# Performance work log

Measured on AMD Instinct MI355X. Metric: run time of the kernel, lower is better.

Reference implementation:

```python
import jax, jax.numpy as jnp
import numpy as np

D_MODEL = 1024
D_STATE = 16
D_CONV = 4
EXPAND = 2
D_INNER = D_MODEL * EXPAND
B = 1
L = 2048


def setup_inputs() -> dict:
    key = jax.random.key(0)
    ks = jax.random.split(key, 8)
    s = lambda k, shape, scale: jax.random.normal(k, shape, dtype=jnp.float32) * scale
    return {
        "x": jax.random.normal(ks[0], (B, L, D_MODEL), dtype=jnp.float32),
        "in_proj_w": s(ks[1], (D_INNER * 2, D_MODEL), D_MODEL ** -0.5),
        "conv_w": s(ks[2], (D_INNER, 1, D_CONV), D_CONV ** -0.5),  # depthwise [O, I/g=1, K]
        "conv_b": jnp.zeros((D_INNER,), jnp.float32),
        "x_proj_w": s(ks[3], (2 * D_STATE + 1, D_INNER), D_INNER ** -0.5),
        "dt_proj_w": s(ks[4], (D_INNER, 1), 1.0),
        "dt_proj_b": jnp.zeros((D_INNER,), jnp.float32),
        "A_log": jnp.log(jnp.broadcast_to(jnp.arange(1, D_STATE + 1, dtype=jnp.float32), (D_INNER, D_STATE))),
        "D": jnp.ones((D_INNER,), jnp.float32),
        "out_proj_w": s(ks[5], (D_MODEL, D_INNER), D_INNER ** -0.5),
    }


def reference(x, in_proj_w, conv_w, conv_b, x_proj_w, dt_proj_w, dt_proj_b, A_log, D, out_proj_w):
    Bb = x.shape[0]
    # in_proj -> split into ssm branch and gate z
    xz = x @ in_proj_w.T                      # [B, L, 2*Di]
    x_ssm, z = jnp.split(xz, 2, axis=-1)
    # causal depthwise conv1d (torch pads K-1 both sides then slices [:L] == left-pad K-1)
    xt = jnp.swapaxes(x_ssm, 1, 2)            # [B, Di, L]
    xc = jax.lax.conv_general_dilated(
        xt, conv_w, window_strides=(1,), padding=[(D_CONV - 1, 0)],
        feature_group_count=D_INNER, dimension_numbers=("NCH", "OIH", "NCH"))
    xc = xc + conv_b[None, :, None]
    xc = jax.nn.silu(jnp.swapaxes(xc, 1, 2))  # [B, L, Di]
    # selective SSM
    A = -jnp.exp(A_log)                        # [Di, N]
    xp = xc @ x_proj_w.T                       # [B, L, 1+2N]
    dt_r = xp[..., :1]
    Bv = xp[..., 1:1 + D_STATE]                # [B, L, N]
    Cv = xp[..., 1 + D_STATE:]                 # [B, L, N]
    dt = jax.nn.softplus(dt_r @ dt_proj_w.T + dt_proj_b)   # [B, L, Di]
    dA = jnp.exp(dt[..., None] * A)                          # [B, L, Di, N]
    dBx = dt[..., None] * Bv[:, :, None, :] * xc[..., None]  # [B, L, Di, N]

    def step(h, inps):
        dA_t, dBx_t, C_t = inps
        h = dA_t * h + dBx_t                   # [B, Di, N]
        y = jnp.einsum("bdn,bn->bd", h, C_t)
        return h, y

    h0 = jnp.zeros((Bb, D_INNER, D_STATE), x.dtype)
    _, ys = jax.lax.scan(step, h0, (jnp.swapaxes(dA, 0, 1), jnp.swapaxes(dBx, 0, 1), jnp.swapaxes(Cv, 0, 1)))
    y = jnp.swapaxes(ys, 0, 1) + xc * D        # [B, L, Di]
    return (y * jax.nn.silu(z)) @ out_proj_w.T
```

## Files before the change

kernel.cpp:

```cpp
#include <hip/hip_runtime.h>
#include <math.h>

#define L_SEQ   2048
#define DM      1024
#define DI      2048
#define NST     16
#define LC      32
#define NCHUNK  64
#define XP_LD   36
#define KSPLIT  8
#define LOG2E   1.44269504f

typedef short s16x8 __attribute__((ext_vector_type(8)));
typedef unsigned short u16x8 __attribute__((ext_vector_type(8)));
typedef float f32x4 __attribute__((ext_vector_type(4)));

__device__ __forceinline__ float silu_f(float x) {
  return x / (1.0f + __expf(-x));
}
__device__ __forceinline__ float softplus_f(float x) {
  return x > 20.0f ? x : __logf(1.0f + __expf(x));
}
__device__ __forceinline__ ushort f2bf(float f) {
  unsigned int u = __float_as_uint(f);
  unsigned int r = (u + 0x7fffu + ((u >> 16) & 1u)) >> 16;
  return (ushort)r;
}
__device__ __forceinline__ float bf2f(ushort u) {
  return __uint_as_float((unsigned int)u << 16);
}
__device__ __forceinline__ void gload_lds16(const void* g, void* lds) {
  __builtin_amdgcn_global_load_lds(
      (const __attribute__((address_space(1))) unsigned int*)g,
      (__attribute__((address_space(3))) unsigned int*)lds,
      16, 0, 0);
}

__global__ __launch_bounds__(256) void cvt_bf16_k(
    const float* __restrict__ in, ushort* __restrict__ out, int n4) {
  int i = blockIdx.x * 256 + threadIdx.x;
  if (i >= n4) return;
  float4 v = ((const float4*)in)[i];
  ushort4 o;
  o.x = f2bf(v.x); o.y = f2bf(v.y); o.z = f2bf(v.z); o.w = f2bf(v.w);
  ((ushort4*)out)[i] = o;
}

template <int MFRAG, bool BF16OUT>
__global__ __launch_bounds__(256) void gemm_mfma_bf16(
    const ushort* __restrict__ A, const ushort* __restrict__ B,
    void* __restrict__ Cv, int K, int ldc) {
  constexpr int BM = MFRAG * 32;
  __shared__ ushort As[BM * 32];
  __shared__ ushort Bs[128 * 32];
  const int tid  = threadIdx.x;
  const int lane = tid & 63;
  const int wv   = tid >> 6;
  const int wr   = wv >> 1;
  const int wc   = wv & 1;
  const int m0 = blockIdx.y * BM;
  const int n0 = blockIdx.x * 128;

  f32x4 acc[MFRAG][4] = {};
  const int kc = (tid & 3) * 8;

  for (int k0 = 0; k0 < K; k0 += 32) {
    __syncthreads();
#pragma unroll
    for (int q = 0; q < BM / 64; ++q) {
      int id = q * 256 + tid;
      int m  = id >> 2;
      gload_lds16(A + (size_t)(m0 + m) * K + k0 + kc, (char*)As + id * 16);
    }
#pragma unroll
    for (int q = 0; q < 2; ++q) {
      int id = q * 256 + tid;
      int n  = id >> 2;
      gload_lds16(B + (size_t)(n0 + n) * K + k0 + kc, (char*)Bs + id * 16);
    }
    __syncthreads();

    s16x8 af[MFRAG], bfr[4];
#pragma unroll
    for (int m = 0; m < MFRAG; ++m)
      af[m] = *(const s16x8*)&As[(wr * MFRAG * 16 + m * 16 + (lane & 15)) * 32 + (lane >> 4) * 8];
#pragma unroll
    for (int n = 0; n < 4; ++n)
      bfr[n] = *(const s16x8*)&Bs[(wc * 64 + n * 16 + (lane & 15)) * 32 + (lane >> 4) * 8];
#pragma unroll
    for (int m = 0; m < MFRAG; ++m)
#pragma unroll
      for (int n = 0; n < 4; ++n)
        acc[m][n] = __builtin_amdgcn_mfma_f32_16x16x32_bf16(af[m], bfr[n], acc[m][n], 0, 0, 0);
  }
  const int cr = (lane >> 4) * 4;
  const int cc = lane & 15;
#pragma unroll
  for (int m = 0; m < MFRAG; ++m) {
    int gr0 = m0 + wr * MFRAG * 16 + m * 16 + cr;
#pragma unroll
    for (int n = 0; n < 4; ++n) {
      int gc = n0 + wc * 64 + n * 16 + cc;
#pragma unroll
      for (int r = 0; r < 4; ++r) {
        if constexpr (BF16OUT)
          ((ushort*)Cv)[(size_t)(gr0 + r) * ldc + gc] = f2bf(acc[m][n][r]);
        else
          ((float*)Cv)[(size_t)(gr0 + r) * ldc + gc] = acc[m][n][r];
      }
    }
  }
}

__global__ __launch_bounds__(256) void conv_silu_T_k(
    const ushort* __restrict__ xzb, const float* __restrict__ cw,
    const float* __restrict__ cb, float* __restrict__ xcT) {
  const int d0  = blockIdx.x * 64;
  const int l0  = blockIdx.y * 64;
  const int tid = threadIdx.x;
  __shared__ ushort xt[67][64];
  __shared__ float  ot[64][65];
#pragma unroll
  for (int q = 0; q < 3; ++q) {
    int id = q * 256 + tid;
    if (id < 67 * 8) {
      int row = id >> 3, c8 = (id & 7) * 8;
      int l = l0 - 3 + row;
      u16x8 v = (u16x8)(ushort)0;
      if (l >= 0)
        v = *(const u16x8*)&xzb[(size_t)l * 4096 + d0 + c8];
      *(u16x8*)&xt[row][c8] = v;
    }
  }
  __syncthreads();
  const int dloc = tid & 63;
  const int d    = d0 + dloc;
  const float w0 = cw[d*4+0], w1 = cw[d*4+1], w2 = cw[d*4+2], w3 = cw[d*4+3];
  const float bb = cb[d];
  const int lb = (tid >> 6) * 16;
#pragma unroll
  for (int j = 0; j < 16; ++j) {
    int ll = lb + j;
    float a = bb;
    a = fmaf(w0, bf2f(xt[ll+0][dloc]), a);
    a = fmaf(w1, bf2f(xt[ll+1][dloc]), a);
    a = fmaf(w2, bf2f(xt[ll+2][dloc]), a);
    a = fmaf(w3, bf2f(xt[ll+3][dloc]), a);
    ot[dloc][ll] = silu_f(a);
  }
  __syncthreads();
#pragma unroll
  for (int q = 0; q < 4; ++q) {
    int f4 = q * 256 + tid;
    int dr = f4 >> 4, lc = (f4 & 15) * 4;
    float4 v = make_float4(ot[dr][lc], ot[dr][lc+1], ot[dr][lc+2], ot[dr][lc+3]);
    *(float4*)&xcT[(size_t)(d0 + dr) * L_SEQ + l0 + lc] = v;
  }
}

__global__ __launch_bounds__(256) void gemm_xp_k(
    const float* __restrict__ xcT, const float* __restrict__ Wxp,
    float* __restrict__ xp_part) {
  const int L0   = blockIdx.x * 64;
  const int ks   = blockIdx.y;
  const int wv   = threadIdx.x >> 6;
  const int lane = threadIdx.x & 63;
  __shared__ float xcs[64][65];
  __shared__ float Ws[36][64];
  float acc[9] = {};
  const int kbeg = ks * (DI / KSPLIT);
  const int kend = kbeg + DI / KSPLIT;
  for (int k0 = kbeg; k0 < kend; k0 += 64) {
#pragma unroll
    for (int q = 0; q < 4; ++q) {
      int f4 = q * 256 + threadIdx.x;
      int dr = f4 >> 4;
      int lc = (f4 & 15) * 4;
      float4 v = *(const float4*)&xcT[(size_t)(k0 + dr) * L_SEQ + L0 + lc];
      xcs[lc+0][dr] = v.x; xcs[lc+1][dr] = v.y;
      xcs[lc+2][dr] = v.z; xcs[lc+3][dr] = v.w;
    }
    for (int idx = threadIdx.x; idx < 36 * 16; idx += 256) {
      int j = idx >> 4; int cc = (idx & 15) << 2;
      float4 v = make_float4(0.f, 0.f, 0.f, 0.f);
      if (j < 33) v = *(const float4*)&Wxp[(size_t)j * DI + k0 + cc];
      *(float4*)&Ws[j][cc] = v;
    }
    __syncthreads();
#pragma unroll 4
    for (int kk = 0; kk < 64; kk += 4) {
      float4 wr[9];
#pragma unroll
      for (int jj = 0; jj < 9; ++jj) wr[jj] = *(const float4*)&Ws[wv*9 + jj][kk];
      float a0 = xcs[lane][kk+0], a1 = xcs[lane][kk+1];
      float a2 = xcs[lane][kk+2], a3 = xcs[lane][kk+3];
#pragma unroll
      for (int jj = 0; jj < 9; ++jj) {
        acc[jj] = fmaf(a0, wr[jj].x, acc[jj]);
        acc[jj] = fmaf(a1, wr[jj].y, acc[jj]);
        acc[jj] = fmaf(a2, wr[jj].z, acc[jj]);
        acc[jj] = fmaf(a3, wr[jj].w, acc[jj]);
      }
    }
    __syncthreads();
  }
  const int l = L0 + lane;
#pragma unroll
  for (int jj = 0; jj < 9; ++jj) {
    int j = wv * 9 + jj;
    if (j < 33)
      xp_part[(size_t)ks * L_SEQ * XP_LD + (size_t)l * XP_LD + j] = acc[jj];
  }
}

__global__ __launch_bounds__(256) void reduce_xp_k(
    const float* __restrict__ part, float* __restrict__ xp) {
  int i = blockIdx.x * 256 + threadIdx.x;
  float s = 0.f;
#pragma unroll
  for (int ks = 0; ks < KSPLIT; ++ks)
    s += part[(size_t)ks * L_SEQ * XP_LD + i];
  xp[i] = s;
}

__device__ __forceinline__ void stage_xps(
    float (*xps)[36], const float* __restrict__ xp, int l0, int tid) {
  for (int idx = tid; idx < LC * 33; idx += 256) {
    int rr = idx / 33, j = idx - rr * 33;
    int col = (j == 0) ? 32 : j - 1;
    xps[rr][col] = xp[(size_t)(l0 + rr) * XP_LD + j];
  }
}
__device__ __forceinline__ void stage_xcs(
    float (*xcs)[LC + 1], const float* __restrict__ xcT, int d0, int l0, int tid) {
#pragma unroll
  for (int q = 0; q < 4; ++q) {
    int f4  = q * 256 + tid;
    int row = f4 >> 3;
    int col = (f4 & 7) * 4;
    float4 v = *(const float4*)&xcT[(size_t)(d0 + row) * L_SEQ + l0 + col];
    xcs[row][col+0] = v.x; xcs[row][col+1] = v.y;
    xcs[row][col+2] = v.z; xcs[row][col+3] = v.w;
  }
}
__device__ __forceinline__ void stage_dts(
    float (*dts)[128], float (*xps)[36],
    const float* __restrict__ dtw, const float* __restrict__ dtb,
    int d0, int tid) {
  int dd = tid & 127;
  int tb = (tid >> 7) * 16;
  float wv = dtw[d0 + dd], bv = dtb[d0 + dd];
#pragma unroll
  for (int j = 0; j < 16; ++j)
    dts[tb + j][dd] = softplus_f(fmaf(xps[tb + j][32], wv, bv));
}

__global__ __launch_bounds__(256) void scan_partial_k(
    const float* __restrict__ xcT, const float* __restrict__ xp,
    const float* __restrict__ dtw, const float* __restrict__ dtb,
    const float* __restrict__ A_log,
    float* __restrict__ P, float* __restrict__ Q) {
  const int tid = threadIdx.x;
  const int dl  = tid >> 1;
  const int d0  = blockIdx.x * 128;
  const int d   = d0 + dl;
  const int nb  = (tid & 1) * 8;
  const int c   = blockIdx.y;
  const int l0  = c * LC;
  __shared__ float xps[LC][36];
  __shared__ float xcs[128][LC + 1];
  __shared__ float dts[LC][128];
  stage_xps(xps, xp, l0, tid);
  stage_xcs(xcs, xcT, d0, l0, tid);

  float Ad2[8];
#pragma unroll
  for (int j4 = 0; j4 < 8; j4 += 4) {
    float4 v = *(const float4*)&A_log[(size_t)d * NST + nb + j4];
    Ad2[j4+0] = -__expf(v.x) * LOG2E; Ad2[j4+1] = -__expf(v.y) * LOG2E;
    Ad2[j4+2] = -__expf(v.z) * LOG2E; Ad2[j4+3] = -__expf(v.w) * LOG2E;
  }
  __syncthreads();
  stage_dts(dts, xps, dtw, dtb, d0, tid);
  float h[8];
#pragma unroll
  for (int n = 0; n < 8; ++n) h[n] = 0.f;
  float sumdt = 0.f;
  __syncthreads();
#pragma unroll 4
  for (int t = 0; t < LC; ++t) {
    float dt  = dts[t][dl];
    sumdt += dt;
    float dtx = dt * xcs[dl][t];
    f32x4 B0 = *(const f32x4*)&xps[t][nb];
    f32x4 B1 = *(const f32x4*)&xps[t][nb + 4];
    float Bv[8];
    *(f32x4*)&Bv[0] = B0; *(f32x4*)&Bv[4] = B1;
#pragma unroll
    for (int n = 0; n < 8; ++n) {
      float da = exp2f(dt * Ad2[n]);
      h[n] = fmaf(da, h[n], dtx * Bv[n]);
    }
  }
  float p[8];
#pragma unroll
  for (int n = 0; n < 8; ++n) p[n] = exp2f(sumdt * Ad2[n]);
  size_t base = ((size_t)c * DI + d) * NST + nb;
  *(float4*)&P[base]     = make_float4(p[0], p[1], p[2], p[3]);
  *(float4*)&P[base + 4] = make_float4(p[4], p[5], p[6], p[7]);
  *(float4*)&Q[base]     = make_float4(h[0], h[1], h[2], h[3]);
  *(float4*)&Q[base + 4] = make_float4(h[4], h[5], h[6], h[7]);
}

__global__ __launch_bounds__(256) void scan_prefix_k(
    const float* __restrict__ P, float* __restrict__ QHs) {
  const int g = blockIdx.x * 256 + threadIdx.x;
  const int d = g >> 2;
  const int q = (g & 3) << 2;
  float4 h = make_float4(0.f, 0.f, 0.f, 0.f);
#pragma unroll 8
  for (int c = 0; c < NCHUNK; ++c) {
    size_t base = ((size_t)c * DI + d) * NST + q;
    float4 pv = *(const float4*)&P[base];
    float4 qv = *(const float4*)&QHs[base];
    *(float4*)&QHs[base] = h;
    h.x = fmaf(pv.x, h.x, qv.x);
    h.y = fmaf(pv.y, h.y, qv.y);
    h.z = fmaf(pv.z, h.z, qv.z);
    h.w = fmaf(pv.w, h.w, qv.w);
  }
}

__global__ __launch_bounds__(256) void scan_final_k(
    const float* __restrict__ xcT, const float* __restrict__ xp,
    const float* __restrict__ dtw, const float* __restrict__ dtb,
    const float* __restrict__ A_log, const float* __restrict__ Dp,
    const float* __restrict__ Hs, const ushort* __restrict__ xzb,
    ushort* __restrict__ ys) {
  const int tid  = threadIdx.x;
  const int dl   = tid >> 1;
  const int d0   = blockIdx.x * 128;
  const int d    = d0 + dl;
  const int half = tid & 1;
  const int nb   = half * 8;
  const int c    = blockIdx.y;
  const int l0   = c * LC;
  __shared__ float  xps[LC][36];
  __shared__ float  xcs[128][LC + 1];
  __shared__ float  dts[LC][128];
  __shared__ ushort zs[LC][128];
#pragma unroll
  for (int q = 0; q < 2; ++q) {
    int id = q * 256 + tid;
    int t  = id >> 4;
    int c8 = (id & 15) * 8;
    gload_lds16(xzb + (size_t)(l0 + t) * 4096 + 2048 + d0 + c8,
                (char*)zs + id * 16);
  }
  stage_xps(xps, xp, l0, tid);
  stage_xcs(xcs, xcT, d0, l0, tid);

  float Ad2[8];
#pragma unroll
  for (int j4 = 0; j4 < 8; j4 += 4) {
    float4 v = *(const float4*)&A_log[(size_t)d * NST + nb + j4];
    Ad2[j4+0] = -__expf(v.x) * LOG2E; Ad2[j4+1] = -__expf(v.y) * LOG2E;
    Ad2[j4+2] = -__expf(v.z) * LOG2E; Ad2[j4+3] = -__expf(v.w) * LOG2E;
  }
  const float Dd = Dp[d];
  float h[8];
  size_t hb = ((size_t)c * DI + d) * NST + nb;
  *(float4*)&h[0] = *(const float4*)&Hs[hb];
  *(float4*)&h[4] = *(const float4*)&Hs[hb + 4];
  __syncthreads();
  stage_dts(dts, xps, dtw, dtb, d0, tid);
  __syncthreads();
#pragma unroll 4
  for (int t = 0; t < LC; ++t) {
    const int l = l0 + t;
    float dt  = dts[t][dl];
    float xcv = xcs[dl][t];
    float dtx = dt * xcv;
    f32x4 B0 = *(const f32x4*)&xps[t][nb];
    f32x4 B1 = *(const f32x4*)&xps[t][nb + 4];
    f32x4 C0 = *(const f32x4*)&xps[t][16 + nb];
    f32x4 C1 = *(const f32x4*)&xps[t][20 + nb];
    float Bv[8], Cv[8];
    *(f32x4*)&Bv[0] = B0; *(f32x4*)&Bv[4] = B1;
    *(f32x4*)&Cv[0] = C0; *(f32x4*)&Cv[4] = C1;
    float y = 0.f;
#pragma unroll
    for (int n = 0; n < 8; ++n) {
      float da = exp2f(dt * Ad2[n]);
      h[n] = fmaf(da, h[n], dtx * Bv[n]);
      y = fmaf(h[n], Cv[n], y);
    }
    y += __shfl_xor(y, 1);
    if (half == 0) {
      y = fmaf(xcv, Dd, y);
      ys[(size_t)l * DI + d] = f2bf(y * silu_f(bf2f(zs[t][dl])));
    }
  }
}

extern "C" void kernel_launch(void* const* d_in, const int* in_sizes, int n_in,
                              void* d_out, int out_size, void* d_ws, size_t ws_size,
                              hipStream_t stream) {
  const float* x    = (const float*)d_in[0];
  const float* W1   = (const float*)d_in[1];
  const float* cw   = (const float*)d_in[2];
  const float* cb   = (const float*)d_in[3];
  const float* Wxp  = (const float*)d_in[4];
  const float* dtw  = (const float*)d_in[5];
  const float* dtb  = (const float*)d_in[6];
  const float* Alog = (const float*)d_in[7];
  const float* Dp   = (const float*)d_in[8];
  const float* Wout = (const float*)d_in[9];
  float* out = (float*)d_out;

  char* w = (char*)d_ws;
  ushort* xz_bf   = (ushort*)w;
  float*  xcT     = (float*)(w + 16777216);
  ushort* x_bf    = (ushort*)(w + 33554432);
  ushort* W1_bf   = (ushort*)(w + 37748736);
  float*  P       = (float*)(w + 33554432);
  float*  QHs     = (float*)(w + 41943040);
  float*  xp      = (float*)(w + 50331648);
  ushort* Wout_bf = (ushort*)(w + 50626560);
  ushort* ys_bf   = (ushort*)(w + 54820864);
  float*  xp_part = (float*)(w + 54820864);

  cvt_bf16_k<<<2048, 256, 0, stream>>>(x,    x_bf,    2048*1024/4);
  cvt_bf16_k<<<4096, 256, 0, stream>>>(W1,   W1_bf,   4096*1024/4);
  cvt_bf16_k<<<2048, 256, 0, stream>>>(Wout, Wout_bf, 1024*2048/4);
  gemm_mfma_bf16<4, true><<<dim3(4096/128, 2048/128), 256, 0, stream>>>(
      x_bf, W1_bf, xz_bf, DM, 4096);
  conv_silu_T_k<<<dim3(DI/64, L_SEQ/64), 256, 0, stream>>>(xz_bf, cw, cb, xcT);
  gemm_xp_k<<<dim3(L_SEQ/64, KSPLIT), 256, 0, stream>>>(xcT, Wxp, xp_part);
  reduce_xp_k<<<L_SEQ*XP_LD/256, 256, 0, stream>>>(xp_part, xp);
  scan_partial_k<<<dim3(DI/128, NCHUNK), 256, 0, stream>>>(xcT, xp, dtw, dtb, Alog, P, QHs);
  scan_prefix_k<<<DI*NST/4/256, 256, 0, stream>>>(P, QHs);
  scan_final_k<<<dim3(DI/128, NCHUNK), 256, 0, stream>>>(xcT, xp, dtw, dtb, Alog, Dp, QHs, xz_bf, ys_bf);
  gemm_mfma_bf16<2, false><<<dim3(1024/128, 2048/64), 256, 0, stream>>>(
      ys_bf, Wout_bf, out, DI, 1024);
}
```

Baseline: 264.9 us.

## Split scan state across four lanes per channel and halve channel tile

```diff
diff --git a/kernel.cpp b/kernel.cpp
--- a/kernel.cpp
+++ b/kernel.cpp
@@ -231,10 +231,10 @@
     xps[rr][col] = xp[(size_t)(l0 + rr) * XP_LD + j];
   }
 }
-__device__ __forceinline__ void stage_xcs(
+__device__ __forceinline__ void stage_xcs64(
     float (*xcs)[LC + 1], const float* __restrict__ xcT, int d0, int l0, int tid) {
 #pragma unroll
-  for (int q = 0; q < 4; ++q) {
+  for (int q = 0; q < 2; ++q) {
     int f4  = q * 256 + tid;
     int row = f4 >> 3;
     int col = (f4 & 7) * 4;
@@ -243,48 +243,41 @@
     xcs[row][col+2] = v.z; xcs[row][col+3] = v.w;
   }
 }
-__device__ __forceinline__ void stage_dts(
-    float (*dts)[128], float (*xps)[36],
+__device__ __forceinline__ void stage_dts64(
+    float (*dts)[64], const float* __restrict__ xp,
     const float* __restrict__ dtw, const float* __restrict__ dtb,
-    int d0, int tid) {
-  int dd = tid & 127;
-  int tb = (tid >> 7) * 16;
+    int d0, int l0, int tid) {
+  int dd = tid & 63;
+  int tb = (tid >> 6) * 8;
   float wv = dtw[d0 + dd], bv = dtb[d0 + dd];
 #pragma unroll
-  for (int j = 0; j < 16; ++j)
-    dts[tb + j][dd] = softplus_f(fmaf(xps[tb + j][32], wv, bv));
-}
-
-__global__ __launch_bounds__(256) void scan_partial_k(
+  for (int j = 0; j < 8; ++j)
+    dts[tb + j][dd] = softplus_f(fmaf(xp[(size_t)(l0 + tb + j) * XP_LD], wv, bv));
+}
+
+__global__ __launch_bounds__(256, 4) void scan_partial_k(
     const float* __restrict__ xcT, const float* __restrict__ xp,
     const float* __restrict__ dtw, const float* __restrict__ dtb,
     const float* __restrict__ A_log,
     float* __restrict__ P, float* __restrict__ Q) {
   const int tid = threadIdx.x;
-  const int dl  = tid >> 1;
-  const int d0  = blockIdx.x * 128;
+  const int dl  = tid >> 2;
+  const int nq  = (tid & 3) * 4;
+  const int d0  = blockIdx.x * 64;
   const int d   = d0 + dl;
-  const int nb  = (tid & 1) * 8;
   const int c   = blockIdx.y;
   const int l0  = c * LC;
   __shared__ float xps[LC][36];
-  __shared__ float xcs[128][LC + 1];
-  __shared__ float dts[LC][128];
+  __shared__ float xcs[64][LC + 1];
+  __shared__ float dts[LC][64];
   stage_xps(xps, xp, l0, tid);
-  stage_xcs(xcs, xcT, d0, l0, tid);
-
-  float Ad2[8];
-#pragma unroll
-  for (int j4 = 0; j4 < 8; j4 += 4) {
-    float4 v = *(const float4*)&A_log[(size_t)d * NST + nb + j4];
-    Ad2[j4+0] = -__expf(v.x) * LOG2E; Ad2[j4+1] = -__expf(v.y) * LOG2E;
-    Ad2[j4+2] = -__expf(v.z) * LOG2E; Ad2[j4+3] = -__expf(v.w) * LOG2E;
-  }
-  __syncthreads();
-  stage_dts(dts, xps, dtw, dtb, d0, tid);
-  float h[8];
-#pragma unroll
-  for (int n = 0; n < 8; ++n) h[n] = 0.f;
+  stage_xcs64(xcs, xcT, d0, l0, tid);
+  stage_dts64(dts, xp, dtw, dtb, d0, l0, tid);
+
+  float4 Av = *(const float4*)&A_log[(size_t)d * NST + nq];
+  float Ad2[4] = { -__expf(Av.x) * LOG2E, -__expf(Av.y) * LOG2E,
+                   -__expf(Av.z) * LOG2E, -__expf(Av.w) * LOG2E };
+  float h[4] = {0.f, 0.f, 0.f, 0.f};
   float sumdt = 0.f;
   __syncthreads();
 #pragma unroll 4
@@ -292,24 +285,17 @@
     float dt  = dts[t][dl];
     sumdt += dt;
     float dtx = dt * xcs[dl][t];
-    f32x4 B0 = *(const f32x4*)&xps[t][nb];
-    f32x4 B1 = *(const f32x4*)&xps[t][nb + 4];
-    float Bv[8];
-    *(f32x4*)&Bv[0] = B0; *(f32x4*)&Bv[4] = B1;
-#pragma unroll
-    for (int n = 0; n < 8; ++n) {
+    f32x4 B = *(const f32x4*)&xps[t][nq];
+#pragma unroll
+    for (int n = 0; n < 4; ++n) {
       float da = exp2f(dt * Ad2[n]);
-      h[n] = fmaf(da, h[n], dtx * Bv[n]);
-    }
-  }
-  float p[8];
-#pragma unroll
-  for (int n = 0; n < 8; ++n) p[n] = exp2f(sumdt * Ad2[n]);
-  size_t base = ((size_t)c * DI + d) * NST + nb;
-  *(float4*)&P[base]     = make_float4(p[0], p[1], p[2], p[3]);
-  *(float4*)&P[base + 4] = make_float4(p[4], p[5], p[6], p[7]);
-  *(float4*)&Q[base]     = make_float4(h[0], h[1], h[2], h[3]);
-  *(float4*)&Q[base + 4] = make_float4(h[4], h[5], h[6], h[7]);
+      h[n] = fmaf(da, h[n], dtx * B[n]);
+    }
+  }
+  size_t base = ((size_t)c * DI + d) * NST + nq;
+  *(float4*)&P[base] = make_float4(exp2f(sumdt * Ad2[0]), exp2f(sumdt * Ad2[1]),
+                                   exp2f(sumdt * Ad2[2]), exp2f(sumdt * Ad2[3]));
+  *(float4*)&Q[base] = make_float4(h[0], h[1], h[2], h[3]);
 }
 
 __global__ __launch_bounds__(256) void scan_prefix_k(
@@ -331,49 +317,41 @@
   }
 }
 
-__global__ __launch_bounds__(256) void scan_final_k(
+__global__ __launch_bounds__(256, 4) void scan_final_k(
     const float* __restrict__ xcT, const float* __restrict__ xp,
     const float* __restrict__ dtw, const float* __restrict__ dtb,
     const float* __restrict__ A_log, const float* __restrict__ Dp,
     const float* __restrict__ Hs, const ushort* __restrict__ xzb,
     ushort* __restrict__ ys) {
-  const int tid  = threadIdx.x;
-  const int dl   = tid >> 1;
-  const int d0   = blockIdx.x * 128;
-  const int d    = d0 + dl;
-  const int half = tid & 1;
-  const int nb   = half * 8;
-  const int c    = blockIdx.y;
-  const int l0   = c * LC;
+  const int tid = threadIdx.x;
+  const int dl  = tid >> 2;
+  const int nq  = (tid & 3) * 4;
+  const int d0  = blockIdx.x * 64;
+  const int d   = d0 + dl;
+  const int c   = blockIdx.y;
+  const int l0  = c * LC;
   __shared__ float  xps[LC][36];
-  __shared__ float  xcs[128][LC + 1];
-  __shared__ float  dts[LC][128];
-  __shared__ ushort zs[LC][128];
-#pragma unroll
-  for (int q = 0; q < 2; ++q) {
-    int id = q * 256 + tid;
-    int t  = id >> 4;
-    int c8 = (id & 15) * 8;
+  __shared__ float  xcs[64][LC + 1];
+  __shared__ float  dts[LC][64];
+  __shared__ ushort zs[LC][64];
+  {
+    int id = tid;
+    int t  = id >> 3;
+    int c8 = (id & 7) * 8;
     gload_lds16(xzb + (size_t)(l0 + t) * 4096 + 2048 + d0 + c8,
                 (char*)zs + id * 16);
   }
   stage_xps(xps, xp, l0, tid);
-  stage_xcs(xcs, xcT, d0, l0, tid);
-
-  float Ad2[8];
-#pragma unroll
-  for (int j4 = 0; j4 < 8; j4 += 4) {
-    float4 v = *(const float4*)&A_log[(size_t)d * NST + nb + j4];
-    Ad2[j4+0] = -__expf(v.x) * LOG2E; Ad2[j4+1] = -__expf(v.y) * LOG2E;
-    Ad2[j4+2] = -__expf(v.z) * LOG2E; Ad2[j4+3] = -__expf(v.w) * LOG2E;
-  }
+  stage_xcs64(xcs, xcT, d0, l0, tid);
+  stage_dts64(dts, xp, dtw, dtb, d0, l0, tid);
+
+  float4 Av = *(const float4*)&A_log[(size_t)d * NST + nq];
+  float Ad2[4] = { -__expf(Av.x) * LOG2E, -__expf(Av.y) * LOG2E,
+                   -__expf(Av.z) * LOG2E, -__expf(Av.w) * LOG2E };
   const float Dd = Dp[d];
-  float h[8];
-  size_t hb = ((size_t)c * DI + d) * NST + nb;
+  float h[4];
+  size_t hb = ((size_t)c * DI + d) * NST + nq;
   *(float4*)&h[0] = *(const float4*)&Hs[hb];
-  *(float4*)&h[4] = *(const float4*)&Hs[hb + 4];
-  __syncthreads();
-  stage_dts(dts, xps, dtw, dtb, d0, tid);
   __syncthreads();
 #pragma unroll 4
   for (int t = 0; t < LC; ++t) {
@@ -381,22 +359,18 @@
     float dt  = dts[t][dl];
     float xcv = xcs[dl][t];
     float dtx = dt * xcv;
-    f32x4 B0 = *(const f32x4*)&xps[t][nb];
-    f32x4 B1 = *(const f32x4*)&xps[t][nb + 4];
-    f32x4 C0 = *(const f32x4*)&xps[t][16 + nb];
-    f32x4 C1 = *(const f32x4*)&xps[t][20 + nb];
-    float Bv[8], Cv[8];
-    *(f32x4*)&Bv[0] = B0; *(f32x4*)&Bv[4] = B1;
-    *(f32x4*)&Cv[0] = C0; *(f32x4*)&Cv[4] = C1;
+    f32x4 B = *(const f32x4*)&xps[t][nq];
+    f32x4 C = *(const f32x4*)&xps[t][16 + nq];
     float y = 0.f;
 #pragma unroll
-    for (int n = 0; n < 8; ++n) {
+    for (int n = 0; n < 4; ++n) {
       float da = exp2f(dt * Ad2[n]);
-      h[n] = fmaf(da, h[n], dtx * Bv[n]);
-      y = fmaf(h[n], Cv[n], y);
+      h[n] = fmaf(da, h[n], dtx * B[n]);
+      y = fmaf(h[n], C[n], y);
     }
     y += __shfl_xor(y, 1);
-    if (half == 0) {
+    y += __shfl_xor(y, 2);
+    if ((tid & 3) == 0) {
       y = fmaf(xcv, Dd, y);
       ys[(size_t)l * DI + d] = f2bf(y * silu_f(bf2f(zs[t][dl])));
     }
@@ -438,9 +412,9 @@
   conv_silu_T_k<<<dim3(DI/64, L_SEQ/64), 256, 0, stream>>>(xz_bf, cw, cb, xcT);
   gemm_xp_k<<<dim3(L_SEQ/64, KSPLIT), 256, 0, stream>>>(xcT, Wxp, xp_part);
   reduce_xp_k<<<L_SEQ*XP_LD/256, 256, 0, stream>>>(xp_part, xp);
-  scan_partial_k<<<dim3(DI/128, NCHUNK), 256, 0, stream>>>(xcT, xp, dtw, dtb, Alog, P, QHs);
+  scan_partial_k<<<dim3(DI/64, NCHUNK), 256, 0, stream>>>(xcT, xp, dtw, dtb, Alog, P, QHs);
   scan_prefix_k<<<DI*NST/4/256, 256, 0, stream>>>(P, QHs);
-  scan_final_k<<<dim3(DI/128, NCHUNK), 256, 0, stream>>>(xcT, xp, dtw, dtb, Alog, Dp, QHs, xz_bf, ys_bf);
+  scan_final_k<<<dim3(DI/64, NCHUNK), 256, 0, stream>>>(xcT, xp, dtw, dtb, Alog, Dp, QHs, xz_bf, ys_bf);
   gemm_mfma_bf16<2, false><<<dim3(1024/128, 2048/64), 256, 0, stream>>>(
       ys_bf, Wout_bf, out, DI, 1024);
 }
```

Result: no change. 263.3 us (-0.6%).
